# Kernel tuning notes

Measured on AMD Instinct MI355X. Metric: run time of the kernel, lower is better.

Reference implementation:

```python
import jax, jax.numpy as jnp
import numpy as np

B, F, D = 16384, 40, 64  # batch, num_fields, embedding_size
D_OUT = 64               # att_embedding_size * head_num = 32 * 2


def setup_inputs() -> dict:
    key = jax.random.key(0)
    ks = jax.random.split(key, 5)
    return {
        "inputs": jax.random.normal(ks[0], (B, F, D), dtype=jnp.float32),
        "W_Query": jax.random.normal(ks[1], (D, D_OUT), dtype=jnp.float32) * 0.05,
        "W_key": jax.random.normal(ks[2], (D, D_OUT), dtype=jnp.float32) * 0.05,
        "W_Value": jax.random.normal(ks[3], (D, D_OUT), dtype=jnp.float32) * 0.05,
        "W_Res": jax.random.normal(ks[4], (D, D_OUT), dtype=jnp.float32) * 0.05,
    }


def reference(inputs, W_Query, W_key, W_Value, W_Res):
    # QKV projections (no head splitting, per original module)
    q = jnp.einsum('bfd,de->bfe', inputs, W_Query)  # [B, F, D_OUT]
    k = jnp.einsum('bfd,de->bfe', inputs, W_key)
    v = jnp.einsum('bfd,de->bfe', inputs, W_Value)
    # scaled-dot-product over the field axis; scaling=False so no divide
    scores = jax.nn.softmax(jnp.einsum('bqe,bke->bqk', q, k), axis=-1)  # [B, F, F]
    result = jnp.einsum('bqk,bke->bqe', scores, v)
    # residual projection (use_res=True)
    result = result + jnp.einsum('bfd,de->bfe', inputs, W_Res)
    return jax.nn.relu(result)
```

## Files before the change

### kernel.cpp

```cpp
#include <hip/hip_runtime.h>
#include <hip/hip_bf16.h>

#define BB  16384
#define F   40
#define D   64
#define E   64
#define LDQ 72
#define LDV 56

typedef __bf16 bf16;
typedef __bf16 bf16x8 __attribute__((ext_vector_type(8)));
typedef __bf16 bf16x4 __attribute__((ext_vector_type(4)));
typedef float  f32x4  __attribute__((ext_vector_type(4)));


__global__ __launch_bounds__(256)
void prep_weights(const float* __restrict__ Wq, const float* __restrict__ Wk,
                  const float* __restrict__ Wv, const float* __restrict__ Wr,
                  bf16* __restrict__ ws)
{
    __shared__ float Gs[64 * 64];
    const int tid = threadIdx.x;
    for (int i = tid; i < 64 * 64; i += 256) {
        int dd = i >> 6, ee = i & 63;
        float s = 0.f;
        for (int e = 0; e < 64; ++e) s += Wq[dd * 64 + e] * Wk[ee * 64 + e];
        Gs[i] = s;
    }
    __syncthreads();
    for (int f = tid; f < 4096; f += 256) {
        int j = f & 7, lane = (f >> 3) & 63, kt = (f >> 9) & 1, nt = f >> 10;
        int dd = kt * 32 + (lane >> 4) * 8 + j;
        int ee = nt * 16 + (lane & 15);
        ws[f]        = (bf16)Gs[dd * 64 + ee];
        ws[4096 + f] = (bf16)Wv[dd * 64 + ee];
        ws[8192 + f] = (bf16)Wr[dd * 64 + ee];
    }
}

__global__ __launch_bounds__(64, 3)
void attn_fused(const float* __restrict__ X,
                const bf16* __restrict__ wfrag,
                float* __restrict__ Out)
{
    __shared__ bf16 QB[48 * LDQ];
    __shared__ bf16 VT[64 * LDV + 16];

    const int lane = threadIdx.x;
    const int l16  = lane & 15;
    const int quad = lane >> 4;
    const int b    = blockIdx.x;
    const float* Xb = X + (size_t)b * (F * D);

    {
        bf16x8 z = {};
        *(bf16x8*)&VT[lane * LDV + 48] = z;
        if (lane < 2) *(bf16x8*)&VT[64 * LDV + lane * 8] = z;
    }

    bf16x8 xf[3][2];
    #pragma unroll
    for (int mt = 0; mt < 3; ++mt) {
        int row = mt * 16 + l16; if (row >= F) row = F - 1;
        #pragma unroll
        for (int kt = 0; kt < 2; ++kt) {
            const float* p = Xb + row * D + kt * 32 + quad * 8;
            float4 u0 = *(const float4*)p;
            float4 u1 = *(const float4*)(p + 4);
            bf16x8 f;
            f[0] = (bf16)u0.x; f[1] = (bf16)u0.y; f[2] = (bf16)u0.z; f[3] = (bf16)u0.w;
            f[4] = (bf16)u1.x; f[5] = (bf16)u1.y; f[6] = (bf16)u1.z; f[7] = (bf16)u1.w;
            xf[mt][kt] = f;
        }
    }

    const bf16x8* gF = (const bf16x8*)wfrag;
    const bf16x8* vF = (const bf16x8*)(wfrag + 4096);
    const bf16x8* rF = (const bf16x8*)(wfrag + 8192);

    f32x4 racc[3][4];
    #pragma unroll
    for (int nt = 0; nt < 4; ++nt) {
        bf16x8 b0 = gF ? rF[(nt * 2 + 0) * 64 + lane] : bf16x8{};
        bf16x8 b1 = rF[(nt * 2 + 1) * 64 + lane];
        #pragma unroll
        for (int mt = 0; mt < 3; ++mt) {
            f32x4 acc = {0.f, 0.f, 0.f, 0.f};
            acc = __builtin_amdgcn_mfma_f32_16x16x32_bf16(xf[mt][0], b0, acc, 0, 0, 0);
            acc = __builtin_amdgcn_mfma_f32_16x16x32_bf16(xf[mt][1], b1, acc, 0, 0, 0);
            racc[mt][nt] = acc;
        }
    }

    #pragma unroll
    for (int nt = 0; nt < 4; ++nt) {
        bf16x8 b0 = vF[(nt * 2 + 0) * 64 + lane];
        bf16x8 b1 = vF[(nt * 2 + 1) * 64 + lane];
        #pragma unroll
        for (int mt = 0; mt < 3; ++mt) {
            f32x4 acc = {0.f, 0.f, 0.f, 0.f};
            acc = __builtin_amdgcn_mfma_f32_16x16x32_bf16(xf[mt][0], b0, acc, 0, 0, 0);
            acc = __builtin_amdgcn_mfma_f32_16x16x32_bf16(xf[mt][1], b1, acc, 0, 0, 0);
            int col = nt * 16 + l16;
            int r0  = mt * 16 + quad * 4;
            bf16x4 pk;
            pk[0] = (bf16)acc[0]; pk[1] = (bf16)acc[1];
            pk[2] = (bf16)acc[2]; pk[3] = (bf16)acc[3];
            *(bf16x4*)&VT[col * LDV + r0] = pk;
        }
    }

    #pragma unroll
    for (int nt = 0; nt < 4; ++nt) {
        bf16x8 b0 = gF[(nt * 2 + 0) * 64 + lane];
        bf16x8 b1 = gF[(nt * 2 + 1) * 64 + lane];
        #pragma unroll
        for (int mt = 0; mt < 3; ++mt) {
            f32x4 acc = {0.f, 0.f, 0.f, 0.f};
            acc = __builtin_amdgcn_mfma_f32_16x16x32_bf16(xf[mt][0], b0, acc, 0, 0, 0);
            acc = __builtin_amdgcn_mfma_f32_16x16x32_bf16(xf[mt][1], b1, acc, 0, 0, 0);
            int col = nt * 16 + l16;
            int r0  = mt * 16 + quad * 4;
            #pragma unroll
            for (int r = 0; r < 4; ++r) QB[(r0 + r) * LDQ + col] = (bf16)acc[r];
        }
    }

    bf16x8 qf[3][2];
    #pragma unroll
    for (int mt = 0; mt < 3; ++mt)
        #pragma unroll
        for (int kt = 0; kt < 2; ++kt)
            qf[mt][kt] = *(const bf16x8*)&QB[(mt * 16 + l16) * LDQ + kt * 32 + quad * 8];
    f32x4 sacc[3][3];
    #pragma unroll
    for (int smt = 0; smt < 3; ++smt)
        #pragma unroll
        for (int snt = 0; snt < 3; ++snt) {
            f32x4 acc = {0.f, 0.f, 0.f, 0.f};
            acc = __builtin_amdgcn_mfma_f32_16x16x32_bf16(qf[smt][0], xf[snt][0], acc, 0, 0, 0);
            acc = __builtin_amdgcn_mfma_f32_16x16x32_bf16(qf[smt][1], xf[snt][1], acc, 0, 0, 0);
            sacc[smt][snt] = acc;
        }

    const bool mask2 = (l16 >= 8);
    #pragma unroll
    for (int smt = 0; smt < 3; ++smt) {
        #pragma unroll
        for (int r = 0; r < 4; ++r) {
            float s0 = sacc[smt][0][r];
            float s1 = sacc[smt][1][r];
            float s2 = mask2 ? -1e30f : sacc[smt][2][r];
            float m = fmaxf(fmaxf(s0, s1), s2);
            #pragma unroll
            for (int off = 1; off < 16; off <<= 1)
                m = fmaxf(m, __shfl_xor(m, off, 64));
            float e0 = __expf(s0 - m);
            float e1 = __expf(s1 - m);
            float e2 = mask2 ? 0.f : __expf(s2 - m);
            float sum = e0 + e1 + e2;
            #pragma unroll
            for (int off = 1; off < 16; off <<= 1)
                sum += __shfl_xor(sum, off, 64);
            float inv = 1.0f / sum;
            int row = smt * 16 + quad * 4 + r;
            if (row < F) {
                QB[row * LDQ + l16]      = (bf16)(e0 * inv);
                QB[row * LDQ + 16 + l16] = (bf16)(e1 * inv);
                QB[row * LDQ + 32 + l16] = (bf16)(e2 * inv);
                QB[row * LDQ + 48 + l16] = (bf16)0.f;
            }
        }
    }

    bf16x8 pf[3][2];
    #pragma unroll
    for (int mt = 0; mt < 3; ++mt)
        #pragma unroll
        for (int kt = 0; kt < 2; ++kt)
            pf[mt][kt] = *(const bf16x8*)&QB[(mt * 16 + l16) * LDQ + kt * 32 + quad * 8];
    #pragma unroll
    for (int nt = 0; nt < 4; ++nt) {
        bf16x8 v0 = *(const bf16x8*)&VT[(nt * 16 + l16) * LDV + 0  + quad * 8];
        bf16x8 v1 = *(const bf16x8*)&VT[(nt * 16 + l16) * LDV + 32 + quad * 8];
        #pragma unroll
        for (int mt = 0; mt < 3; ++mt) {
            f32x4 acc = racc[mt][nt];
            acc = __builtin_amdgcn_mfma_f32_16x16x32_bf16(pf[mt][0], v0, acc, 0, 0, 0);
            acc = __builtin_amdgcn_mfma_f32_16x16x32_bf16(pf[mt][1], v1, acc, 0, 0, 0);
            int col = nt * 16 + l16;
            #pragma unroll
            for (int r = 0; r < 4; ++r) {
                int row = mt * 16 + quad * 4 + r;
                if (row < F)
                    Out[(size_t)b * (F * E) + row * E + col] = fmaxf(acc[r], 0.f);
            }
        }
    }
}

extern "C" void kernel_launch(void* const* d_in, const int* in_sizes, int n_in,
                              void* d_out, int out_size, void* d_ws, size_t ws_size,
                              hipStream_t stream) {
    const float* X  = (const float*)d_in[0];
    const float* Wq = (const float*)d_in[1];
    const float* Wk = (const float*)d_in[2];
    const float* Wv = (const float*)d_in[3];
    const float* Wr = (const float*)d_in[4];
    float* Out = (float*)d_out;
    bf16* ws = (bf16*)d_ws;

    prep_weights<<<1, 256, 0, stream>>>(Wq, Wk, Wv, Wr, ws);
    attn_fused<<<BB, 64, 0, stream>>>(X, ws, Out);
}
```

Baseline: 380.3 us.

## Process several batches per block with X prefetch and drop softmax max pass

The attention kernel now handles four batch elements per workgroup, prefetching the next element's inputs into registers while computing the current one. Softmax skips the row-max reduction, the residual projection is fused into the final MFMA chain to free registers, and the weight prep kernel uses MFMA across three blocks. This aims to hide global load latency and cut shuffle work, but dropping the max subtraction risks exp overflow for large scores, and fewer blocks reduces parallelism.

```diff
diff --git a/kernel.cpp b/kernel.cpp
--- a/kernel.cpp
+++ b/kernel.cpp
@@ -1,199 +1,226 @@
 #include <hip/hip_runtime.h>
 #include <hip/hip_bf16.h>
 
-#define BB  16384
-#define F   40
-#define D   64
-#define E   64
-#define LDQ 72
-#define LDV 56
+#define BB   16384
+#define F    40
+#define LDQ  72
+#define LDV  56
+#define ITER 4
 
 typedef __bf16 bf16;
 typedef __bf16 bf16x8 __attribute__((ext_vector_type(8)));
 typedef __bf16 bf16x4 __attribute__((ext_vector_type(4)));
 typedef float  f32x4  __attribute__((ext_vector_type(4)));
 
+
+__device__ __forceinline__ bf16x8 cvt8(float4 a, float4 b) {
+    bf16x8 f;
+    f[0] = (bf16)a.x; f[1] = (bf16)a.y; f[2] = (bf16)a.z; f[3] = (bf16)a.w;
+    f[4] = (bf16)b.x; f[5] = (bf16)b.y; f[6] = (bf16)b.z; f[7] = (bf16)b.w;
+    return f;
+}
 
 __global__ __launch_bounds__(256)
 void prep_weights(const float* __restrict__ Wq, const float* __restrict__ Wk,
                   const float* __restrict__ Wv, const float* __restrict__ Wr,
                   bf16* __restrict__ ws)
 {
+    const int tid = threadIdx.x;
+    if (blockIdx.x > 0) {
+        const float* W = (blockIdx.x == 1) ? Wv : Wr;
+        bf16* dst = ws + 4096 * blockIdx.x;
+        for (int f = tid; f < 4096; f += 256) {
+            int j = f & 7, ln = (f >> 3) & 63, kt = (f >> 9) & 1, nt = f >> 10;
+            dst[f] = (bf16)W[(kt * 32 + (ln >> 4) * 8 + j) * 64 + nt * 16 + (ln & 15)];
+        }
+        return;
+    }
     __shared__ float Gs[64 * 64];
-    const int tid = threadIdx.x;
-    for (int i = tid; i < 64 * 64; i += 256) {
-        int dd = i >> 6, ee = i & 63;
-        float s = 0.f;
-        for (int e = 0; e < 64; ++e) s += Wq[dd * 64 + e] * Wk[ee * 64 + e];
-        Gs[i] = s;
+    if (tid < 64) {
+        const int l16 = tid & 15, quad = tid >> 4;
+        bf16x8 aq[4][2], ak[4][2];
+        #pragma unroll
+        for (int mt = 0; mt < 4; ++mt)
+            #pragma unroll
+            for (int kt = 0; kt < 2; ++kt) {
+                const float* pq = Wq + (mt * 16 + l16) * 64 + kt * 32 + quad * 8;
+                const float* pk = Wk + (mt * 16 + l16) * 64 + kt * 32 + quad * 8;
+                aq[mt][kt] = cvt8(*(const float4*)pq, *(const float4*)(pq + 4));
+                ak[mt][kt] = cvt8(*(const float4*)pk, *(const float4*)(pk + 4));
+            }
+        #pragma unroll
+        for (int mt = 0; mt < 4; ++mt)
+            #pragma unroll
+            for (int nt = 0; nt < 4; ++nt) {
+                f32x4 acc = {0.f, 0.f, 0.f, 0.f};
+                acc = __builtin_amdgcn_mfma_f32_16x16x32_bf16(aq[mt][0], ak[nt][0], acc, 0, 0, 0);
+                acc = __builtin_amdgcn_mfma_f32_16x16x32_bf16(aq[mt][1], ak[nt][1], acc, 0, 0, 0);
+                #pragma unroll
+                for (int r = 0; r < 4; ++r)
+                    Gs[(mt * 16 + quad * 4 + r) * 64 + nt * 16 + l16] = acc[r];
+            }
     }
     __syncthreads();
     for (int f = tid; f < 4096; f += 256) {
-        int j = f & 7, lane = (f >> 3) & 63, kt = (f >> 9) & 1, nt = f >> 10;
-        int dd = kt * 32 + (lane >> 4) * 8 + j;
-        int ee = nt * 16 + (lane & 15);
-        ws[f]        = (bf16)Gs[dd * 64 + ee];
-        ws[4096 + f] = (bf16)Wv[dd * 64 + ee];
-        ws[8192 + f] = (bf16)Wr[dd * 64 + ee];
+        int j = f & 7, ln = (f >> 3) & 63, kt = (f >> 9) & 1, nt = f >> 10;
+        ws[f] = (bf16)Gs[(kt * 32 + (ln >> 4) * 8 + j) * 64 + nt * 16 + (ln & 15)];
     }
 }
 
 __global__ __launch_bounds__(64, 3)
-void attn_fused(const float* __restrict__ X,
-                const bf16* __restrict__ wfrag,
+void attn_fused(const float* __restrict__ X, const bf16* __restrict__ wfrag,
                 float* __restrict__ Out)
 {
-    __shared__ bf16 QB[48 * LDQ];
-    __shared__ bf16 VT[64 * LDV + 16];
+    __shared__ bf16 QB[40 * LDQ];
+    __shared__ bf16 VT[64 * LDV + 8];
 
     const int lane = threadIdx.x;
     const int l16  = lane & 15;
     const int quad = lane >> 4;
-    const int b    = blockIdx.x;
-    const float* Xb = X + (size_t)b * (F * D);
 
     {
         bf16x8 z = {};
         *(bf16x8*)&VT[lane * LDV + 48] = z;
-        if (lane < 2) *(bf16x8*)&VT[64 * LDV + lane * 8] = z;
-    }
-
-    bf16x8 xf[3][2];
-    #pragma unroll
-    for (int mt = 0; mt < 3; ++mt) {
-        int row = mt * 16 + l16; if (row >= F) row = F - 1;
-        #pragma unroll
-        for (int kt = 0; kt < 2; ++kt) {
-            const float* p = Xb + row * D + kt * 32 + quad * 8;
-            float4 u0 = *(const float4*)p;
-            float4 u1 = *(const float4*)(p + 4);
-            bf16x8 f;
-            f[0] = (bf16)u0.x; f[1] = (bf16)u0.y; f[2] = (bf16)u0.z; f[3] = (bf16)u0.w;
-            f[4] = (bf16)u1.x; f[5] = (bf16)u1.y; f[6] = (bf16)u1.z; f[7] = (bf16)u1.w;
-            xf[mt][kt] = f;
-        }
+        if (lane == 0) *(bf16x8*)&VT[64 * LDV] = z;
     }
 
     const bf16x8* gF = (const bf16x8*)wfrag;
-    const bf16x8* vF = (const bf16x8*)(wfrag + 4096);
-    const bf16x8* rF = (const bf16x8*)(wfrag + 8192);
-
-    f32x4 racc[3][4];
-    #pragma unroll
-    for (int nt = 0; nt < 4; ++nt) {
-        bf16x8 b0 = gF ? rF[(nt * 2 + 0) * 64 + lane] : bf16x8{};
-        bf16x8 b1 = rF[(nt * 2 + 1) * 64 + lane];
+    const bf16x8* vF = gF + 512;
+    const bf16x8* rF = gF + 1024;
+
+    const size_t b0 = (size_t)blockIdx.x * ITER;
+
+    float4 pA[3][2], pB[3][2];
+    {
+        const float* Xb = X + b0 * (F * 64);
         #pragma unroll
         for (int mt = 0; mt < 3; ++mt) {
-            f32x4 acc = {0.f, 0.f, 0.f, 0.f};
-            acc = __builtin_amdgcn_mfma_f32_16x16x32_bf16(xf[mt][0], b0, acc, 0, 0, 0);
-            acc = __builtin_amdgcn_mfma_f32_16x16x32_bf16(xf[mt][1], b1, acc, 0, 0, 0);
-            racc[mt][nt] = acc;
-        }
-    }
-
-    #pragma unroll
-    for (int nt = 0; nt < 4; ++nt) {
-        bf16x8 b0 = vF[(nt * 2 + 0) * 64 + lane];
-        bf16x8 b1 = vF[(nt * 2 + 1) * 64 + lane];
+            int row = mt * 16 + l16; if (row >= F) row = F - 1;
+            #pragma unroll
+            for (int kt = 0; kt < 2; ++kt) {
+                const float* p = Xb + row * 64 + kt * 32 + quad * 8;
+                pA[mt][kt] = *(const float4*)p;
+                pB[mt][kt] = *(const float4*)(p + 4);
+            }
+        }
+    }
+
+    #pragma unroll 1
+    for (int it = 0; it < ITER; ++it) {
+        bf16x8 xf[3][2];
+        #pragma unroll
+        for (int mt = 0; mt < 3; ++mt)
+            #pragma unroll
+            for (int kt = 0; kt < 2; ++kt)
+                xf[mt][kt] = cvt8(pA[mt][kt], pB[mt][kt]);
+
+        if (it + 1 < ITER) {
+            const float* Xb = X + (b0 + it + 1) * (F * 64);
+            #pragma unroll
+            for (int mt = 0; mt < 3; ++mt) {
+                int row = mt * 16 + l16; if (row >= F) row = F - 1;
+                #pragma unroll
+                for (int kt = 0; kt < 2; ++kt) {
+                    const float* p = Xb + row * 64 + kt * 32 + quad * 8;
+                    pA[mt][kt] = *(const float4*)p;
+                    pB[mt][kt] = *(const float4*)(p + 4);
+                }
+            }
+        }
+
+        #pragma unroll
+        for (int nt = 0; nt < 4; ++nt) {
+            bf16x8 g0 = gF[(nt * 2 + 0) * 64 + lane];
+            bf16x8 g1 = gF[(nt * 2 + 1) * 64 + lane];
+            #pragma unroll
+            for (int mt = 0; mt < 3; ++mt) {
+                f32x4 acc = {0.f, 0.f, 0.f, 0.f};
+                acc = __builtin_amdgcn_mfma_f32_16x16x32_bf16(xf[mt][0], g0, acc, 0, 0, 0);
+                acc = __builtin_amdgcn_mfma_f32_16x16x32_bf16(xf[mt][1], g1, acc, 0, 0, 0);
+                int col = nt * 16 + l16, r0 = mt * 16 + quad * 4;
+                #pragma unroll
+                for (int r = 0; r < 4; ++r)
+                    if (r0 + r < F) QB[(r0 + r) * LDQ + col] = (bf16)acc[r];
+            }
+        }
+
+        #pragma unroll
+        for (int nt = 0; nt < 4; ++nt) {
+            bf16x8 v0 = vF[(nt * 2 + 0) * 64 + lane];
+            bf16x8 v1 = vF[(nt * 2 + 1) * 64 + lane];
+            #pragma unroll
+            for (int mt = 0; mt < 3; ++mt) {
+                f32x4 acc = {0.f, 0.f, 0.f, 0.f};
+                acc = __builtin_amdgcn_mfma_f32_16x16x32_bf16(xf[mt][0], v0, acc, 0, 0, 0);
+                acc = __builtin_amdgcn_mfma_f32_16x16x32_bf16(xf[mt][1], v1, acc, 0, 0, 0);
+                bf16x4 pk;
+                pk[0] = (bf16)acc[0]; pk[1] = (bf16)acc[1];
+                pk[2] = (bf16)acc[2]; pk[3] = (bf16)acc[3];
+                *(bf16x4*)&VT[(nt * 16 + l16) * LDV + mt * 16 + quad * 4] = pk;
+            }
+        }
+
+        const bool mask2 = (l16 >= 8);
+        #pragma unroll
+        for (int smt = 0; smt < 3; ++smt) {
+            int qrow = smt * 16 + l16; if (qrow >= F) qrow = F - 1;
+            bf16x8 q0 = *(const bf16x8*)&QB[qrow * LDQ + 0  + quad * 8];
+            bf16x8 q1 = *(const bf16x8*)&QB[qrow * LDQ + 32 + quad * 8];
+            f32x4 sa[3];
+            #pragma unroll
+            for (int snt = 0; snt < 3; ++snt) {
+                f32x4 acc = {0.f, 0.f, 0.f, 0.f};
+                acc = __builtin_amdgcn_mfma_f32_16x16x32_bf16(q0, xf[snt][0], acc, 0, 0, 0);
+                acc = __builtin_amdgcn_mfma_f32_16x16x32_bf16(q1, xf[snt][1], acc, 0, 0, 0);
+                sa[snt] = acc;
+            }
+            #pragma unroll
+            for (int r = 0; r < 4; ++r) {
+                float e0 = __expf(sa[0][r]);
+                float e1 = __expf(sa[1][r]);
+                float e2 = mask2 ? 0.f : __expf(sa[2][r]);
+                float sum = e0 + e1 + e2;
+                #pragma unroll
+                for (int off = 1; off < 16; off <<= 1)
+                    sum += __shfl_xor(sum, off, 64);
+                float inv = 1.0f / sum;
+                int row = smt * 16 + quad * 4 + r;
+                if (row < F) {
+                    QB[row * LDQ + l16]      = (bf16)(e0 * inv);
+                    QB[row * LDQ + 16 + l16] = (bf16)(e1 * inv);
+                    QB[row * LDQ + 32 + l16] = (bf16)(e2 * inv);
+                    QB[row * LDQ + 48 + l16] = (bf16)0.f;
+                }
+            }
+        }
+
+        bf16x8 pf[3][2];
         #pragma unroll
         for (int mt = 0; mt < 3; ++mt) {
-            f32x4 acc = {0.f, 0.f, 0.f, 0.f};
-            acc = __builtin_amdgcn_mfma_f32_16x16x32_bf16(xf[mt][0], b0, acc, 0, 0, 0);
-            acc = __builtin_amdgcn_mfma_f32_16x16x32_bf16(xf[mt][1], b1, acc, 0, 0, 0);
-            int col = nt * 16 + l16;
-            int r0  = mt * 16 + quad * 4;
-            bf16x4 pk;
-            pk[0] = (bf16)acc[0]; pk[1] = (bf16)acc[1];
-            pk[2] = (bf16)acc[2]; pk[3] = (bf16)acc[3];
-            *(bf16x4*)&VT[col * LDV + r0] = pk;
-        }
-    }
-
-    #pragma unroll
-    for (int nt = 0; nt < 4; ++nt) {
-        bf16x8 b0 = gF[(nt * 2 + 0) * 64 + lane];
-        bf16x8 b1 = gF[(nt * 2 + 1) * 64 + lane];
-        #pragma unroll
-        for (int mt = 0; mt < 3; ++mt) {
-            f32x4 acc = {0.f, 0.f, 0.f, 0.f};
-            acc = __builtin_amdgcn_mfma_f32_16x16x32_bf16(xf[mt][0], b0, acc, 0, 0, 0);
-            acc = __builtin_amdgcn_mfma_f32_16x16x32_bf16(xf[mt][1], b1, acc, 0, 0, 0);
-            int col = nt * 16 + l16;
-            int r0  = mt * 16 + quad * 4;
-            #pragma unroll
-            for (int r = 0; r < 4; ++r) QB[(r0 + r) * LDQ + col] = (bf16)acc[r];
-        }
-    }
-
-    bf16x8 qf[3][2];
-    #pragma unroll
-    for (int mt = 0; mt < 3; ++mt)
-        #pragma unroll
-        for (int kt = 0; kt < 2; ++kt)
-            qf[mt][kt] = *(const bf16x8*)&QB[(mt * 16 + l16) * LDQ + kt * 32 + quad * 8];
-    f32x4 sacc[3][3];
-    #pragma unroll
-    for (int smt = 0; smt < 3; ++smt)
-        #pragma unroll
-        for (int snt = 0; snt < 3; ++snt) {
-            f32x4 acc = {0.f, 0.f, 0.f, 0.f};
-            acc = __builtin_amdgcn_mfma_f32_16x16x32_bf16(qf[smt][0], xf[snt][0], acc, 0, 0, 0);
-            acc = __builtin_amdgcn_mfma_f32_16x16x32_bf16(qf[smt][1], xf[snt][1], acc, 0, 0, 0);
-            sacc[smt][snt] = acc;
-        }
-
-    const bool mask2 = (l16 >= 8);
-    #pragma unroll
-    for (int smt = 0; smt < 3; ++smt) {
-        #pragma unroll
-        for (int r = 0; r < 4; ++r) {
-            float s0 = sacc[smt][0][r];
-            float s1 = sacc[smt][1][r];
-            float s2 = mask2 ? -1e30f : sacc[smt][2][r];
-            float m = fmaxf(fmaxf(s0, s1), s2);
-            #pragma unroll
-            for (int off = 1; off < 16; off <<= 1)
-                m = fmaxf(m, __shfl_xor(m, off, 64));
-            float e0 = __expf(s0 - m);
-            float e1 = __expf(s1 - m);
-            float e2 = mask2 ? 0.f : __expf(s2 - m);
-            float sum = e0 + e1 + e2;
-            #pragma unroll
-            for (int off = 1; off < 16; off <<= 1)
-                sum += __shfl_xor(sum, off, 64);
-            float inv = 1.0f / sum;
-            int row = smt * 16 + quad * 4 + r;
-            if (row < F) {
-                QB[row * LDQ + l16]      = (bf16)(e0 * inv);
-                QB[row * LDQ + 16 + l16] = (bf16)(e1 * inv);
-                QB[row * LDQ + 32 + l16] = (bf16)(e2 * inv);
-                QB[row * LDQ + 48 + l16] = (bf16)0.f;
-            }
-        }
-    }
-
-    bf16x8 pf[3][2];
-    #pragma unroll
-    for (int mt = 0; mt < 3; ++mt)
-        #pragma unroll
-        for (int kt = 0; kt < 2; ++kt)
-            pf[mt][kt] = *(const bf16x8*)&QB[(mt * 16 + l16) * LDQ + kt * 32 + quad * 8];
-    #pragma unroll
-    for (int nt = 0; nt < 4; ++nt) {
-        bf16x8 v0 = *(const bf16x8*)&VT[(nt * 16 + l16) * LDV + 0  + quad * 8];
-        bf16x8 v1 = *(const bf16x8*)&VT[(nt * 16 + l16) * LDV + 32 + quad * 8];
-        #pragma unroll
-        for (int mt = 0; mt < 3; ++mt) {
-            f32x4 acc = racc[mt][nt];
-            acc = __builtin_amdgcn_mfma_f32_16x16x32_bf16(pf[mt][0], v0, acc, 0, 0, 0);
-            acc = __builtin_amdgcn_mfma_f32_16x16x32_bf16(pf[mt][1], v1, acc, 0, 0, 0);
-            int col = nt * 16 + l16;
-            #pragma unroll
-            for (int r = 0; r < 4; ++r) {
-                int row = mt * 16 + quad * 4 + r;
-                if (row < F)
-                    Out[(size_t)b * (F * E) + row * E + col] = fmaxf(acc[r], 0.f);
+            int prow = mt * 16 + l16; if (prow >= F) prow = F - 1;
+            pf[mt][0] = *(const bf16x8*)&QB[prow * LDQ + 0  + quad * 8];
+            pf[mt][1] = *(const bf16x8*)&QB[prow * LDQ + 32 + quad * 8];
+        }
+        #pragma unroll
+        for (int nt = 0; nt < 4; ++nt) {
+            bf16x8 r0f = rF[(nt * 2 + 0) * 64 + lane];
+            bf16x8 r1f = rF[(nt * 2 + 1) * 64 + lane];
+            bf16x8 v0  = *(const bf16x8*)&VT[(nt * 16 + l16) * LDV + 0  + quad * 8];
+            bf16x8 v1  = *(const bf16x8*)&VT[(nt * 16 + l16) * LDV + 32 + quad * 8];
+            #pragma unroll
+            for (int mt = 0; mt < 3; ++mt) {
+                f32x4 acc = {0.f, 0.f, 0.f, 0.f};
+                acc = __builtin_amdgcn_mfma_f32_16x16x32_bf16(xf[mt][0], r0f, acc, 0, 0, 0);
+                acc = __builtin_amdgcn_mfma_f32_16x16x32_bf16(xf[mt][1], r1f, acc, 0, 0, 0);
+                acc = __builtin_amdgcn_mfma_f32_16x16x32_bf16(pf[mt][0], v0, acc, 0, 0, 0);
+                acc = __builtin_amdgcn_mfma_f32_16x16x32_bf16(pf[mt][1], v1, acc, 0, 0, 0);
+                int col = nt * 16 + l16;
+                #pragma unroll
+                for (int r = 0; r < 4; ++r) {
+                    int row = mt * 16 + quad * 4 + r;
+                    if (row < F)
+                        Out[(b0 + it) * (size_t)(F * 64) + row * 64 + col] = fmaxf(acc[r], 0.f);
+                }
             }
         }
     }
@@ -210,6 +237,6 @@
     float* Out = (float*)d_out;
     bf16* ws = (bf16*)d_ws;
 
-    prep_weights<<<1, 256, 0, stream>>>(Wq, Wk, Wv, Wr, ws);
-    attn_fused<<<BB, 64, 0, stream>>>(X, ws, Out);
-}
+    prep_weights<<<3, 256, 0, stream>>>(Wq, Wk, Wv, Wr, ws);
+    attn_fused<<<BB / ITER, 64, 0, stream>>>(X, ws, Out);
+}
```

Result: slower. 495.9 us (+30.4%).
